# Performance work log

Hardware: AMD Instinct MI355X
Metric: run time of the kernel (lower is better)

## Reference

```python
import math
import jax, jax.numpy as jnp
import numpy as np

CT = {"SDD": 1000.0, "SCD": 500.0, "det_interval": 1.0, "num_det": 736}


def ramp_filter_np(ct, scale):
    # Standard equiangular fan-beam ramp filter (utility.ramp_filter):
    #   h[0] = 1/(8*db^2); h[n odd] = -1/(2*(pi*sin(n*db))^2); h[n even!=0] = 0
    db = ct["det_interval"] / ct["SDD"] * scale  # angular detector pitch at this scale
    n_det = int(ct["num_det"] // scale)
    n = np.arange(-(n_det - 1), n_det)  # length K = 2*n_det - 1
    h = np.zeros(n.shape, dtype=np.float32)
    h[n == 0] = 1.0 / (8.0 * db ** 2)
    odd = (n % 2) != 0
    h[odd] = -0.5 / (np.pi * np.sin(n[odd] * db)) ** 2
    return h


def setup_inputs() -> dict:
    key = jax.random.key(0)
    scale = 1
    batch, ch, view, det = 16, 1, 1152, CT["num_det"] // scale
    sinogram = jax.random.normal(key, (batch, ch, view, det), dtype=jnp.float32)
    delta_b = CT["det_interval"] / CT["SDD"]
    # recon_filter = ramp_filter * scale * delta_b, shaped [1,1,1,K] (OIHW)
    filt = ramp_filter_np(CT, scale) * scale * delta_b
    recon_filter = jnp.asarray(filt, dtype=jnp.float32)[None, None, None, :]
    return {"sinogram": sinogram, "recon_filter": recon_filter, "scale": scale}


def reference(sinogram, recon_filter, scale):
    det = sinogram.shape[-1]
    # cosine fan-beam pre-weighting
    s_range = (CT["det_interval"]
               * jnp.linspace((1.0 - det) / 2.0, (det - 1.0) / 2.0, det, dtype=jnp.float32)
               * scale) / CT["SDD"]
    cos_weight = (CT["SCD"] / 10000.0) * jnp.cos(s_range)  # [det]
    x = sinogram * cos_weight[None, None, None, :]
    # 1D ramp-filter convolution along detector axis (F.conv2d with 1xK kernel)
    K = recon_filter.shape[-1]
    pad = K // 2
    out = jax.lax.conv_general_dilated(
        x, recon_filter,
        window_strides=(1, 1),
        padding=[(0, 0), (pad, pad)],
        dimension_numbers=("NCHW", "OIHW", "NCHW"),
    )
    return out
```

## Files before the change

### kernel.cpp

```cpp
#include <hip/hip_runtime.h>

typedef unsigned short ushort_t;
typedef ushort_t u16x8 __attribute__((ext_vector_type(8)));
typedef __bf16 bf16x8 __attribute__((ext_vector_type(8)));
typedef float f32x4 __attribute__((ext_vector_type(4)));

#define DET 736
#define NPAD 768

__device__ __forceinline__ ushort_t f2bf(float f) {
    unsigned u = __builtin_bit_cast(unsigned, f);
    u += 0x7FFFu + ((u >> 16) & 1u);
    return (ushort_t)(u >> 16);
}

__device__ __forceinline__ void gload16(const void* g, void* l) {
    __builtin_amdgcn_global_load_lds(
        (const __attribute__((address_space(1))) unsigned int*)g,
        (__attribute__((address_space(3))) unsigned int*)l,
        16, 0, 0);
}

__global__ void prep_x(const float* __restrict__ sino, ushort_t* __restrict__ X, int total) {
    int idx = (blockIdx.x * blockDim.x + threadIdx.x) * 4;
    if (idx >= total) return;
    const float4 v = *(const float4*)(sino + idx);
    float vv[4] = {v.x, v.y, v.z, v.w};
    int j = idx % DET;
    ushort_t oo[4];
#pragma unroll
    for (int t = 0; t < 4; ++t) {
        float w = 0.05f * cosf(((float)(j + t) - 367.5f) * 0.001f);
        oo[t] = f2bf(vv[t] * w);
    }
    ushort4 o; o.x = oo[0]; o.y = oo[1]; o.z = oo[2]; o.w = oo[3];
    *(ushort4*)(X + idx) = o;
}

__global__ void prep_bt(const float* __restrict__ filt, ushort_t* __restrict__ Bt) {
    int idx = blockIdx.x * blockDim.x + threadIdx.x;
    if (idx >= NPAD * DET) return;
    int n = idx / DET;
    int k = idx - n * DET;
    float v = (n < DET) ? filt[k - n + (DET - 1)] : 0.0f;
    Bt[idx] = f2bf(v);
}

__global__ __launch_bounds__(256) void gemm_bt(
    const ushort_t* __restrict__ A,
    const ushort_t* __restrict__ Bt,
    float* __restrict__ C, int M)
{
    __shared__ ushort_t As[128 * 32];
    __shared__ ushort_t Bs[128 * 32];

    const int tid  = threadIdx.x;
    const int lane = tid & 63;
    const int warp = tid >> 6;
    const int wm   = warp & 1;
    const int wn   = warp >> 1;
    const int quad = lane >> 4;
    const int l16  = lane & 15;

    const size_t row_a0 = (size_t)blockIdx.x * 128;
    const int    row_b0 = blockIdx.y * 128;

    f32x4 acc[4][4];
#pragma unroll
    for (int i = 0; i < 4; ++i)
#pragma unroll
        for (int jx = 0; jx < 4; ++jx)
            acc[i][jx] = (f32x4){0.f, 0.f, 0.f, 0.f};

    const int c0 = tid, c1 = tid + 256;
    const int r0 = c0 >> 2, q0 = c0 & 3;
    const int r1 = c1 >> 2, q1 = c1 & 3;

    const ushort_t* gA0 = A + (row_a0 + r0) * DET + q0 * 8;
    const ushort_t* gA1 = A + (row_a0 + r1) * DET + q1 * 8;
    const ushort_t* gB0 = Bt + (size_t)(row_b0 + r0) * DET + q0 * 8;
    const ushort_t* gB1 = Bt + (size_t)(row_b0 + r1) * DET + q1 * 8;

    for (int k0 = 0; k0 < DET; k0 += 32) {
        __syncthreads();
        gload16(gA0 + k0, As + c0 * 8);
        gload16(gA1 + k0, As + c1 * 8);
        gload16(gB0 + k0, Bs + c0 * 8);
        gload16(gB1 + k0, Bs + c1 * 8);
        __syncthreads();

        u16x8 af[4], bfr[4];
#pragma unroll
        for (int mi = 0; mi < 4; ++mi)
            af[mi] = *(const u16x8*)(As + (wm * 64 + mi * 16 + l16) * 32 + quad * 8);
#pragma unroll
        for (int ni = 0; ni < 4; ++ni)
            bfr[ni] = *(const u16x8*)(Bs + (wn * 64 + ni * 16 + l16) * 32 + quad * 8);
#pragma unroll
        for (int mi = 0; mi < 4; ++mi)
#pragma unroll
            for (int ni = 0; ni < 4; ++ni)
                acc[mi][ni] = __builtin_amdgcn_mfma_f32_16x16x32_bf16(
                    __builtin_bit_cast(bf16x8, af[mi]),
                    __builtin_bit_cast(bf16x8, bfr[ni]),
                    acc[mi][ni], 0, 0, 0);
    }

#pragma unroll
    for (int mi = 0; mi < 4; ++mi) {
#pragma unroll
        for (int ni = 0; ni < 4; ++ni) {
            int colg = row_b0 + wn * 64 + ni * 16 + l16;
            if (colg < DET) {
#pragma unroll
                for (int r = 0; r < 4; ++r) {
                    size_t rowg = row_a0 + wm * 64 + mi * 16 + quad * 4 + r;
                    C[rowg * DET + colg] = acc[mi][ni][r];
                }
            }
        }
    }
}

extern "C" void kernel_launch(void* const* d_in, const int* in_sizes, int n_in,
                              void* d_out, int out_size, void* d_ws, size_t ws_size,
                              hipStream_t stream) {
    const float* sino = (const float*)d_in[0];
    const float* filt = (const float*)d_in[1];
    int total = in_sizes[0];
    int M = total / DET;

    ushort_t* Xbf = (ushort_t*)d_ws;
    ushort_t* Btb = Xbf + (size_t)total;
    float* out = (float*)d_out;

    prep_x<<<(total / 4 + 255) / 256, 256, 0, stream>>>(sino, Xbf, total);
    prep_bt<<<(NPAD * DET + 255) / 256, 256, 0, stream>>>(filt, Btb);

    dim3 grid(M / 128, NPAD / 128);
    gemm_bt<<<grid, 256, 0, stream>>>(Xbf, Btb, out, M);
}
```

Measured before the change: 139.1 us.

## Fuse cosine weighting into filter matrix and convert sinogram inside GEMM

Removes the separate prep_x pass by folding the per-detector cosine weight into the Toeplitz filter matrix (weight depends only on k). The GEMM now reads fp32 sinogram directly, converts to bf16 in registers and stores to LDS, with the next tile's A loads issued after the barrier to overlap with MFMA work. This removes one kernel launch and a bf16 intermediate round trip, but doubles A global traffic per GEMM block (fp32, re-read across 6 column blocks) and adds register pressure under the new occupancy hint.

```diff
diff --git a/kernel.cpp b/kernel.cpp
--- a/kernel.cpp
+++ b/kernel.cpp
@@ -7,6 +7,7 @@
 
 #define DET 736
 #define NPAD 768
+#define NT 23
 
 __device__ __forceinline__ ushort_t f2bf(float f) {
     unsigned u = __builtin_bit_cast(unsigned, f);
@@ -21,33 +22,18 @@
         16, 0, 0);
 }
 
-__global__ void prep_x(const float* __restrict__ sino, ushort_t* __restrict__ X, int total) {
-    int idx = (blockIdx.x * blockDim.x + threadIdx.x) * 4;
-    if (idx >= total) return;
-    const float4 v = *(const float4*)(sino + idx);
-    float vv[4] = {v.x, v.y, v.z, v.w};
-    int j = idx % DET;
-    ushort_t oo[4];
-#pragma unroll
-    for (int t = 0; t < 4; ++t) {
-        float w = 0.05f * cosf(((float)(j + t) - 367.5f) * 0.001f);
-        oo[t] = f2bf(vv[t] * w);
-    }
-    ushort4 o; o.x = oo[0]; o.y = oo[1]; o.z = oo[2]; o.w = oo[3];
-    *(ushort4*)(X + idx) = o;
-}
-
 __global__ void prep_bt(const float* __restrict__ filt, ushort_t* __restrict__ Bt) {
     int idx = blockIdx.x * blockDim.x + threadIdx.x;
     if (idx >= NPAD * DET) return;
     int n = idx / DET;
     int k = idx - n * DET;
-    float v = (n < DET) ? filt[k - n + (DET - 1)] : 0.0f;
+    float w = 0.05f * cosf(((float)k - 367.5f) * 0.001f);
+    float v = (n < DET) ? filt[k - n + (DET - 1)] * w : 0.0f;
     Bt[idx] = f2bf(v);
 }
 
-__global__ __launch_bounds__(256) void gemm_bt(
-    const ushort_t* __restrict__ A,
+__global__ __launch_bounds__(256, 4) void gemm_fused(
+    const float* __restrict__ A,
     const ushort_t* __restrict__ Bt,
     float* __restrict__ C, int M)
 {
@@ -76,18 +62,43 @@
     const int r0 = c0 >> 2, q0 = c0 & 3;
     const int r1 = c1 >> 2, q1 = c1 & 3;
 
-    const ushort_t* gA0 = A + (row_a0 + r0) * DET + q0 * 8;
-    const ushort_t* gA1 = A + (row_a0 + r1) * DET + q1 * 8;
+    const float*    gA0 = A + (row_a0 + r0) * DET + q0 * 8;
+    const float*    gA1 = A + (row_a0 + r1) * DET + q1 * 8;
     const ushort_t* gB0 = Bt + (size_t)(row_b0 + r0) * DET + q0 * 8;
     const ushort_t* gB1 = Bt + (size_t)(row_b0 + r1) * DET + q1 * 8;
 
-    for (int k0 = 0; k0 < DET; k0 += 32) {
+    f32x4 a0lo = *(const f32x4*)(gA0);
+    f32x4 a0hi = *(const f32x4*)(gA0 + 4);
+    f32x4 a1lo = *(const f32x4*)(gA1);
+    f32x4 a1hi = *(const f32x4*)(gA1 + 4);
+
+    for (int t = 0; t < NT; ++t) {
         __syncthreads();
-        gload16(gA0 + k0, As + c0 * 8);
-        gload16(gA1 + k0, As + c1 * 8);
+
+        u16x8 oa0, oa1;
+#pragma unroll
+        for (int e = 0; e < 4; ++e) {
+            oa0[e]     = f2bf(a0lo[e]);
+            oa0[e + 4] = f2bf(a0hi[e]);
+            oa1[e]     = f2bf(a1lo[e]);
+            oa1[e + 4] = f2bf(a1hi[e]);
+        }
+        *(u16x8*)(As + c0 * 8) = oa0;
+        *(u16x8*)(As + c1 * 8) = oa1;
+
+        const int k0 = t * 32;
         gload16(gB0 + k0, Bs + c0 * 8);
         gload16(gB1 + k0, Bs + c1 * 8);
+
         __syncthreads();
+
+        if (t + 1 < NT) {
+            const int kn = (t + 1) * 32;
+            a0lo = *(const f32x4*)(gA0 + kn);
+            a0hi = *(const f32x4*)(gA0 + kn + 4);
+            a1lo = *(const f32x4*)(gA1 + kn);
+            a1hi = *(const f32x4*)(gA1 + kn + 4);
+        }
 
         u16x8 af[4], bfr[4];
 #pragma unroll
@@ -130,13 +141,11 @@
     int total = in_sizes[0];
     int M = total / DET;
 
-    ushort_t* Xbf = (ushort_t*)d_ws;
-    ushort_t* Btb = Xbf + (size_t)total;
+    ushort_t* Btb = (ushort_t*)d_ws;
     float* out = (float*)d_out;
 
-    prep_x<<<(total / 4 + 255) / 256, 256, 0, stream>>>(sino, Xbf, total);
     prep_bt<<<(NPAD * DET + 255) / 256, 256, 0, stream>>>(filt, Btb);
 
     dim3 grid(M / 128, NPAD / 128);
-    gemm_bt<<<grid, 256, 0, stream>>>(Xbf, Btb, out, M);
+    gemm_fused<<<grid, 256, 0, stream>>>(sino, Btb, out, M);
 }
```

Measured after the change: 132.2 us. 4.9% less time.
